# Kernel optimization log

Measured on AMD Instinct MI355X. Metric: run time of the kernel, lower is better.

Reference implementation:

```python
import jax, jax.numpy as jnp
import numpy as np

DIM = 256
HEADS = 8
HD = DIM // HEADS
SR = 2
SCALE = HD ** -0.5
EPS = 1e-5


def _layernorm(t, g, b):
    m = jnp.mean(t, axis=-1, keepdims=True)
    v = jnp.mean((t - m) ** 2, axis=-1, keepdims=True)
    return (t - m) / jnp.sqrt(v + EPS) * g + b


def _sr_kv(t, H, W, sr_w, sr_b, ln_g, ln_b, Wkv):
    # t: [B, N, C] with N == H*W -> spatial-reduction conv -> LN -> kv proj
    B, N, C = t.shape
    img = t.transpose(0, 2, 1).reshape(B, C, H, W)
    red = jax.lax.conv_general_dilated(
        img, sr_w, window_strides=(SR, SR), padding='VALID',
        dimension_numbers=('NCHW', 'OIHW', 'NCHW')) + sr_b[None, :, None, None]
    red = red.reshape(B, C, -1).transpose(0, 2, 1)  # [B, Nr, C]
    red = _layernorm(red, ln_g, ln_b)
    Nr = red.shape[1]
    kv = (red @ Wkv).reshape(B, Nr, 2, HEADS, HD).transpose(2, 0, 3, 1, 4)
    return kv[0], kv[1]  # k, v: [B, h, Nr, d]


def _q_heads(t, Wq):
    B, N, _ = t.shape
    return (t @ Wq).reshape(B, N, HEADS, HD).transpose(0, 2, 1, 3)  # [B,h,N,d]


def _attn_out(q, k, v, proj_w, proj_b):
    a = jnp.einsum('bhqd,bhkd->bhqk', q, k) * SCALE
    a = jax.nn.softmax(a, axis=-1)
    o = jnp.einsum('bhqk,bhkd->bhqd', a, v)
    B, h, N, d = o.shape
    return o.transpose(0, 2, 1, 3).reshape(B, N, h * d) @ proj_w + proj_b


def _forward(x, y, Wq, Wkv, sr_w, sr_b, ln_g, ln_b, proj_w, proj_b,
             H_x, W_x, H_y, W_y):
    # B_x == 1 branch of the original module (static shapes)
    B_y = y.shape[0]
    q_x = _q_heads(x, Wq)
    q_y = _q_heads(y, Wq)
    k_x, v_x = _sr_kv(x, H_x, W_x, sr_w, sr_b, ln_g, ln_b, Wkv)
    k_y, v_y = _sr_kv(y, H_y, W_y, sr_w, sr_b, ln_g, ln_b, Wkv)
    # x attends to its own KV + batch-averaged support KV
    k_cat_x = jnp.concatenate([k_x, jnp.mean(k_y, axis=0, keepdims=True)], axis=2)
    v_cat_x = jnp.concatenate([v_x, jnp.mean(v_y, axis=0, keepdims=True)], axis=2)
    x_out = _attn_out(q_x, k_cat_x, v_cat_x, proj_w, proj_b)
    # each support attends to repeated query KV + its own KV
    k_cat_y = jnp.concatenate([jnp.broadcast_to(k_x, (B_y,) + k_x.shape[1:]), k_y], axis=2)
    v_cat_y = jnp.concatenate([jnp.broadcast_to(v_x, (B_y,) + v_x.shape[1:]), v_y], axis=2)
    y_out = _attn_out(q_y, k_cat_y, v_cat_y, proj_w, proj_b)
    return x_out, y_out


def setup_inputs() -> dict:
    key = jax.random.key(0)
    ks = jax.random.split(key, 6)
    std = 0.02
    return {
        'x': jax.random.normal(ks[0], (1, 6400, DIM), jnp.float32),
        'y': jax.random.normal(ks[1], (4, 1024, DIM), jnp.float32),
        'Wq': jax.random.normal(ks[2], (DIM, DIM), jnp.float32) * std,
        'Wkv': jax.random.normal(ks[3], (DIM, 2 * DIM), jnp.float32) * std,
        'sr_w': jax.random.normal(ks[4], (DIM, DIM, SR, SR), jnp.float32) * np.sqrt(2.0 / (SR * SR * DIM)),
        'sr_b': jnp.zeros((DIM,), jnp.float32),
        'ln_g': jnp.ones((DIM,), jnp.float32),
        'ln_b': jnp.zeros((DIM,), jnp.float32),
        'proj_w': jax.random.normal(ks[5], (DIM, DIM), jnp.float32) * std,
        'proj_b': jnp.zeros((DIM,), jnp.float32),
        'H_x': 80, 'W_x': 80, 'H_y': 32, 'W_y': 32,
    }


def reference(x, y, Wq, Wkv, sr_w, sr_b, ln_g, ln_b, proj_w, proj_b,
              H_x, W_x, H_y, W_y):
    return _forward(x, y, Wq, Wkv, sr_w, sr_b, ln_g, ln_b, proj_w, proj_b,
                    H_x, W_x, H_y, W_y)
```

## Files before the change

kernel.cpp:

```cpp
#include <hip/hip_runtime.h>
#include <math.h>

#define DIM 256
#define HD 32
#define KSCALE (0.17677669529663687f * 1.44269504088896340736f)
#define EPS 1e-5f

typedef __attribute__((ext_vector_type(8))) short short8;
typedef __attribute__((ext_vector_type(4))) float f32x4;

union U8 { uint4 u; short8 s; };

__device__ inline unsigned short f2bf(float f) {
    union { float f; unsigned u; } v; v.f = f;
    unsigned r = v.u + 0x7FFF + ((v.u >> 16) & 1);
    return (unsigned short)(r >> 16);
}
__device__ inline float bf2f(unsigned short h) {
    union { unsigned u; float f; } v; v.u = ((unsigned)h) << 16;
    return v.f;
}
__device__ inline unsigned pk2bf(float a, float b) {
    unsigned ua = __float_as_uint(a) + 0x8000u;
    unsigned ub = __float_as_uint(b) + 0x8000u;
    return __builtin_amdgcn_perm(ub, ua, 0x07060302u);
}
__device__ inline uint4 pk8bf(float4 a, float4 b) {
    return make_uint4(pk2bf(a.x, a.y), pk2bf(a.z, a.w),
                      pk2bf(b.x, b.y), pk2bf(b.z, b.w));
}
__device__ inline void up2(unsigned u, float& a, float& b) {
    a = __uint_as_float(u << 16);
    b = __uint_as_float(u & 0xffff0000u);
}
__device__ inline void gl_lds16(const unsigned short* g, unsigned short* l) {
    __builtin_amdgcn_global_load_lds(
        (const __attribute__((address_space(1))) unsigned int*)g,
        (__attribute__((address_space(3))) unsigned int*)l, 16, 0, 0);
}
#define MFMA16(a, b, c) __builtin_amdgcn_mfma_f32_16x16x32_bf16(a, b, c, 0, 0, 0)
#define EXP2(x) __builtin_amdgcn_exp2f(x)

__global__ __launch_bounds__(256) void prep_w(
    const float* __restrict__ Wq, const float* __restrict__ Wkv,
    const float* __restrict__ projw, const float* __restrict__ srw,
    unsigned short* __restrict__ WqT, unsigned short* __restrict__ WkvT,
    unsigned short* __restrict__ projT, unsigned short* __restrict__ BwT)
{
    int idx = blockIdx.x * 256 + threadIdx.x;
    if (idx < 65536) { int n = idx >> 8, k = idx & 255; WqT[idx] = f2bf(Wq[(k << 8) + n]); return; }
    idx -= 65536;
    if (idx < 131072) { int n = idx >> 8, k = idx & 255; WkvT[idx] = f2bf(Wkv[(k << 9) + n]); return; }
    idx -= 131072;
    if (idx < 65536) { int n = idx >> 8, k = idx & 255; projT[idx] = f2bf(projw[(k << 8) + n]); return; }
    idx -= 65536;
    { int o = idx >> 10, rem = idx & 1023, q = rem >> 8, i = rem & 255;
      BwT[idx] = f2bf(srw[(o << 10) + (i << 2) + q]); }
}

__global__ __launch_bounds__(256) void convq_kernel(
    const float* __restrict__ x, const float* __restrict__ y,
    const unsigned short* __restrict__ BwT, const float* __restrict__ srb,
    const unsigned short* __restrict__ WqT,
    unsigned short* __restrict__ redx, unsigned short* __restrict__ redy,
    unsigned short* __restrict__ qxb, unsigned short* __restrict__ qyb)
{
    __shared__ __align__(16) unsigned short At[64][32];
    __shared__ __align__(16) unsigned short Btile[64][32];
    const int tid = threadIdx.x;
    const int lane = tid & 63, w = tid >> 6;
    const int c = lane & 15, quad = lane >> 4;
    const int srow = tid >> 2, sch = (tid & 3) << 3;
    const int bid = blockIdx.x;
    f32x4 acc[4] = {};
    const int rl = (w << 4) + (quad << 2);

    if (bid < 164) {
        const int n0 = (bid & 3) << 6, myi = bid >> 2;
        const float* Xb; unsigned short* Cb; int W, W2, m0;
        if (myi < 25) { Xb = x; Cb = redx; W = 80; W2 = 40; m0 = myi * 64; }
        else {
            const int r = myi - 25, b = r >> 2;
            Xb = y + (size_t)b * 262144; Cb = redy + (size_t)b * 65536;
            W = 32; W2 = 16; m0 = (r & 3) * 64;
        }
        const int p = m0 + srow;
        const int oy = p / W2, ox = p - oy * W2;
        const unsigned short* Bp = BwT + (size_t)(n0 + srow) * 1024 + sch;

        auto addrA = [&](int k0) {
            const int qq = k0 >> 8;
            const int rrow = (2 * oy + (qq >> 1)) * W + 2 * ox + (qq & 1);
            return Xb + (size_t)rrow * DIM + (k0 & 255) + sch;
        };

        const float* ap = addrA(0);
        float4 a0 = *(const float4*)ap, a1 = *(const float4*)(ap + 4);
        uint4 bn = *(const uint4*)Bp;
        for (int k0 = 0; k0 < 1024; k0 += 32) {
            *(uint4*)&At[srow][sch]    = pk8bf(a0, a1);
            *(uint4*)&Btile[srow][sch] = bn;
            if (k0 < 992) {
                const float* np = addrA(k0 + 32);
                a0 = *(const float4*)np; a1 = *(const float4*)(np + 4);
                bn = *(const uint4*)(Bp + k0 + 32);
            }
            __syncthreads();
            short8 a = *(short8*)&At[(w << 4) + c][quad << 3];
            #pragma unroll
            for (int nb = 0; nb < 4; ++nb) {
                short8 b = *(short8*)&Btile[(nb << 4) + c][quad << 3];
                acc[nb] = MFMA16(a, b, acc[nb]);
            }
            __syncthreads();
        }
        #pragma unroll
        for (int nb = 0; nb < 4; ++nb) {
            const int col = n0 + (nb << 4) + c;
            const float bv = srb[col];
            #pragma unroll
            for (int r = 0; r < 4; ++r)
                Cb[(size_t)(m0 + rl + r) * DIM + col] = f2bf(acc[nb][r] + bv);
        }
    } else {
        const int r = bid - 164;
        const int n0 = (r & 3) << 6, mg = (r >> 2) << 6;
        const float* Ab = (mg < 6400) ? x + (size_t)mg * 256
                                      : y + (size_t)(mg - 6400) * 256;
        unsigned short* Cb = (mg < 6400) ? qxb + (size_t)mg * 256
                                         : qyb + (size_t)(mg - 6400) * 256;
        const float* Ap = Ab + (size_t)srow * 256 + sch;
        const unsigned short* Bp = WqT + (size_t)(n0 + srow) * 256 + sch;

        float4 a0 = *(const float4*)Ap, a1 = *(const float4*)(Ap + 4);
        uint4 bn = *(const uint4*)Bp;
        for (int k0 = 0; k0 < 256; k0 += 32) {
            *(uint4*)&At[srow][sch]    = pk8bf(a0, a1);
            *(uint4*)&Btile[srow][sch] = bn;
            if (k0 < 224) {
                a0 = *(const float4*)(Ap + k0 + 32);
                a1 = *(const float4*)(Ap + k0 + 36);
                bn = *(const uint4*)(Bp + k0 + 32);
            }
            __syncthreads();
            short8 a = *(short8*)&At[(w << 4) + c][quad << 3];
            #pragma unroll
            for (int nb = 0; nb < 4; ++nb) {
                short8 b = *(short8*)&Btile[(nb << 4) + c][quad << 3];
                acc[nb] = MFMA16(a, b, acc[nb]);
            }
            __syncthreads();
        }
        #pragma unroll
        for (int nb = 0; nb < 4; ++nb) {
            const int col = n0 + (nb << 4) + c;
            #pragma unroll
            for (int r = 0; r < 4; ++r)
                Cb[(size_t)(rl + r) * 256 + col] = f2bf(acc[nb][r]);
        }
    }
}

__global__ __launch_bounds__(256) void kvln_kernel(
    const unsigned short* __restrict__ redx, const unsigned short* __restrict__ redy,
    const unsigned short* __restrict__ WkvT,
    const float* __restrict__ g, const float* __restrict__ bta,
    unsigned short* __restrict__ kswx, unsigned short* __restrict__ vswx,
    unsigned short* __restrict__ kswy, unsigned short* __restrict__ vswy)
{
    __shared__ __align__(16) unsigned short At[64][32];
    __shared__ __align__(16) unsigned short Btile[64][32];
    const int tid = threadIdx.x;
    const int lane = tid & 63, w = tid >> 6;
    const int c = lane & 15, quad = lane >> 4;
    const int srow = tid >> 2, sch = (tid & 3) << 3;
    const int bid = blockIdx.x;
    const int n0 = (bid & 7) << 6, mg = (bid >> 3) << 6;
    const unsigned short* Ab = (mg < 1600) ? redx + (size_t)mg * 256
                                           : redy + (size_t)(mg - 1600) * 256;
    const unsigned short* Arow = Ab + (size_t)srow * 256 + sch;

    uint4 araw[8];
    float s1 = 0.f, s2 = 0.f;
    #pragma unroll
    for (int ci = 0; ci < 8; ++ci) {
        araw[ci] = *(const uint4*)(Arow + (ci << 5));
        const unsigned* du = (const unsigned*)&araw[ci];
        #pragma unroll
        for (int dd = 0; dd < 4; ++dd) {
            float a, b; up2(du[dd], a, b);
            s1 += a + b; s2 += a * a + b * b;
        }
    }
    s1 += __shfl_xor(s1, 1); s1 += __shfl_xor(s1, 2);
    s2 += __shfl_xor(s2, 1); s2 += __shfl_xor(s2, 2);
    const float mean = s1 * (1.0f / 256.0f);
    const float var  = s2 * (1.0f / 256.0f) - mean * mean;
    const float rstd = rsqrtf(var + EPS);

    #pragma unroll
    for (int ci = 0; ci < 8; ++ci) {
        const int ch = (ci << 5) + sch;
        float4 g0 = *(const float4*)(g + ch),   g1 = *(const float4*)(g + ch + 4);
        float4 b0 = *(const float4*)(bta + ch), b1 = *(const float4*)(bta + ch + 4);
        const unsigned* du = (const unsigned*)&araw[ci];
        float v[8];
        #pragma unroll
        for (int dd = 0; dd < 4; ++dd) up2(du[dd], v[2 * dd], v[2 * dd + 1]);
        float4 o0 = make_float4(fmaf((v[0] - mean) * rstd, g0.x, b0.x),
                                fmaf((v[1] - mean) * rstd, g0.y, b0.y),
                                fmaf((v[2] - mean) * rstd, g0.z, b0.z),
                                fmaf((v[3] - mean) * rstd, g0.w, b0.w));
        float4 o1 = make_float4(fmaf((v[4] - mean) * rstd, g1.x, b1.x),
                                fmaf((v[5] - mean) * rstd, g1.y, b1.y),
                                fmaf((v[6] - mean) * rstd, g1.z, b1.z),
                                fmaf((v[7] - mean) * rstd, g1.w, b1.w));
        araw[ci] = pk8bf(o0, o1);
    }

    const unsigned short* Bp = WkvT + (size_t)(n0 + srow) * 256 + sch;
    uint4 bn = *(const uint4*)Bp;
    f32x4 acc[4] = {};
    for (int k0 = 0; k0 < 256; k0 += 32) {
        *(uint4*)&At[srow][sch]    = araw[k0 >> 5];
        *(uint4*)&Btile[srow][sch] = bn;
        if (k0 < 224) bn = *(const uint4*)(Bp + k0 + 32);
        __syncthreads();
        short8 a = *(short8*)&At[(w << 4) + c][quad << 3];
        #pragma unroll
        for (int nb = 0; nb < 4; ++nb) {
            short8 b = *(short8*)&Btile[(nb << 4) + c][quad << 3];
            acc[nb] = MFMA16(a, b, acc[nb]);
        }
        __syncthreads();
    }

    const int rl = (w << 4) + (quad << 2);
    const int r0 = mg - 1600;
    #pragma unroll
    for (int nb = 0; nb < 4; ++nb) {
        const int col = n0 + (nb << 4) + c;
        if (col < 256) {
            const int hh = col >> 5, d = col & 31;
            unsigned short* base = (mg < 1600)
                ? kswx + ((size_t)(hh * 25 + (mg >> 6)) << 11)
                : kswy + ((size_t)(r0 >> 8) << 16) + ((size_t)((hh << 2) + ((r0 >> 6) & 3)) << 11);
            unsigned short* dst = base + (((d >> 3) << 9)) + (d & 7);
            #pragma unroll
            for (int r = 0; r < 4; ++r)
                dst[(rl + r) << 3] = f2bf(acc[nb][r] * KSCALE);
        } else {
            const int hd = col - 256, hv = hd >> 5, d = hd & 31;
            unsigned short* base = (mg < 1600)
                ? vswx + ((size_t)(hv * 25 + (mg >> 6)) << 11)
                : vswy + ((size_t)(r0 >> 8) << 16) + ((size_t)((hv << 2) + ((r0 >> 6) & 3)) << 11);
            const int j0 = ((w >> 1) << 5) + (quad << 3) + ((w & 1) << 2);
            const int kc = j0 >> 5, qq = (j0 >> 3) & 3, u = j0 & 7;
            unsigned lo = (unsigned)f2bf(acc[nb][0]) | ((unsigned)f2bf(acc[nb][1]) << 16);
            unsigned hi = (unsigned)f2bf(acc[nb][2]) | ((unsigned)f2bf(acc[nb][3]) << 16);
            *(uint2*)(base + ((size_t)(((kc << 2) + qq) * 32 + d) << 3) + u) =
                make_uint2(lo, hi);
        }
    }
}

__global__ __launch_bounds__(256) void kvmean_kernel(
    const unsigned short* __restrict__ kswy, const unsigned short* __restrict__ vswy,
    unsigned short* __restrict__ kmsw, unsigned short* __restrict__ vmsw)
{
    int idx = blockIdx.x * 256 + threadIdx.x;
    const unsigned short* s; unsigned short* dv; int e;
    if (idx < 65536) { s = kswy; dv = kmsw; e = idx; }
    else             { s = vswy; dv = vmsw; e = idx - 65536; }
    float sm = bf2f(s[e]) + bf2f(s[e + 65536]) + bf2f(s[e + 131072]) + bf2f(s[e + 196608]);
    dv[e] = f2bf(0.25f * sm);
}

__global__ __launch_bounds__(256) void attn_mfma(
    unsigned short* __restrict__ qxb, unsigned short* __restrict__ qyb,
    const unsigned short* __restrict__ kswx, const unsigned short* __restrict__ vswx,
    const unsigned short* __restrict__ kmsw, const unsigned short* __restrict__ vmsw,
    const unsigned short* __restrict__ kswy, const unsigned short* __restrict__ vswy)
{
    __shared__ __align__(16) unsigned short Kt[2][2048];
    __shared__ __align__(16) unsigned short Vt[2][2048];

    const int tid = threadIdx.x;
    const int lane = tid & 63, w = tid >> 6;
    const int c = lane & 15, quad = lane >> 4;

    const int bid = blockIdx.x;
    unsigned short* qb; const unsigned short *k1, *v1, *k2, *v2;
    int h, qoff;
    if (bid < 800) {
        h = bid / 100; qoff = (bid - h * 100) * 64;
        qb = qxb;
        k1 = kswx + ((size_t)h * 25 << 11); v1 = vswx + ((size_t)h * 25 << 11);
        k2 = kmsw + ((size_t)h << 13);      v2 = vmsw + ((size_t)h << 13);
    } else {
        const int idx = bid - 800, b = idx >> 7, rem = idx & 127;
        h = rem >> 4; qoff = b * 1024 + (rem & 15) * 64;
        qb = qyb;
        k1 = kswx + ((size_t)h * 25 << 11); v1 = vswx + ((size_t)h * 25 << 11);
        k2 = kswy + ((size_t)b << 16) + ((size_t)h << 13);
        v2 = vswy + ((size_t)b << 16) + ((size_t)h << 13);
    }

    const int qrow = qoff + (w << 4) + c;
    const short8 qf = *(const short8*)(qb + (size_t)qrow * DIM + h * HD + (quad << 3));

    const int lel = (w << 9) + (lane << 3);

    auto stage = [&](int t, int pb) {
        const unsigned short *ks, *vs;
        if (t < 25) { ks = k1 + (t << 11); vs = v1 + (t << 11); }
        else        { ks = k2 + ((t - 25) << 11); vs = v2 + ((t - 25) << 11); }
        gl_lds16(ks + lel, &Kt[pb][w << 9]);
        gl_lds16(vs + lel, &Vt[pb][w << 9]);
    };

    float lsr = 0.f;
    f32x4 oacc[2] = {};
    const f32x4 zero = {0.f, 0.f, 0.f, 0.f};

    stage(0, 0);
    __syncthreads();

    for (int t = 0; t < 29; ++t) {
        const int pb = t & 1;
        if (t < 28) stage(t + 1, pb ^ 1);

        const unsigned short* Kp = &Kt[pb][quad << 9];
        f32x4 sacc[4];
        #pragma unroll
        for (int kb = 0; kb < 4; ++kb) {
            short8 ka = *(const short8*)(Kp + (((kb << 4) + c) << 3));
            sacc[kb] = MFMA16(ka, qf, zero);
        }
        float p[16];
        #pragma unroll
        for (int kb = 0; kb < 4; ++kb) {
            p[4 * kb + 0] = EXP2(sacc[kb][0]);
            p[4 * kb + 1] = EXP2(sacc[kb][1]);
            p[4 * kb + 2] = EXP2(sacc[kb][2]);
            p[4 * kb + 3] = EXP2(sacc[kb][3]);
            lsr += (p[4 * kb + 0] + p[4 * kb + 1]) + (p[4 * kb + 2] + p[4 * kb + 3]);
        }
        U8 af0, af1;
        af0.u = make_uint4(pk2bf(p[0], p[1]), pk2bf(p[2], p[3]),
                           pk2bf(p[4], p[5]), pk2bf(p[6], p[7]));
        af1.u = make_uint4(pk2bf(p[8], p[9]), pk2bf(p[10], p[11]),
                           pk2bf(p[12], p[13]), pk2bf(p[14], p[15]));
        const unsigned short* Vp = &Vt[pb][0];
        short8 v00 = *(const short8*)(Vp + (((quad << 5) + c) << 3));
        short8 v01 = *(const short8*)(Vp + (((quad << 5) + 16 + c) << 3));
        short8 v10 = *(const short8*)(Vp + ((((4 + quad) << 5) + c) << 3));
        short8 v11 = *(const short8*)(Vp + ((((4 + quad) << 5) + 16 + c) << 3));
        oacc[0] = MFMA16(af0.s, v00, oacc[0]);
        oacc[1] = MFMA16(af0.s, v01, oacc[1]);
        oacc[0] = MFMA16(af1.s, v10, oacc[0]);
        oacc[1] = MFMA16(af1.s, v11, oacc[1]);

        __syncthreads();
    }

    lsr += __shfl_xor(lsr, 16);
    lsr += __shfl_xor(lsr, 32);

    #pragma unroll
    for (int r = 0; r < 4; ++r) {
        const float inv = 1.0f / __shfl(lsr, (quad << 2) + r);
        const int row = qoff + (w << 4) + (quad << 2) + r;
        qb[(size_t)row * DIM + h * HD + c]      = f2bf(oacc[0][r] * inv);
        qb[(size_t)row * DIM + h * HD + 16 + c] = f2bf(oacc[1][r] * inv);
    }
}

__global__ __launch_bounds__(256) void proj_mfma(
    const unsigned short* __restrict__ qxb, const unsigned short* __restrict__ qyb,
    const unsigned short* __restrict__ projT, const float* __restrict__ bias,
    float* __restrict__ outx, float* __restrict__ outy)
{
    __shared__ __align__(16) unsigned short At[64][32];
    __shared__ __align__(16) unsigned short Btile[64][32];
    const int tid = threadIdx.x;
    const int lane = tid & 63, w = tid >> 6;
    const int c = lane & 15, quad = lane >> 4;
    const int srow = tid >> 2, sch = (tid & 3) << 3;

    const int bid = blockIdx.x;
    const int n0 = (bid & 3) << 6, mg = (bid >> 2) << 6;
    const unsigned short* Ab = (mg < 6400) ? qxb + (size_t)mg * 256
                                           : qyb + (size_t)(mg - 6400) * 256;
    float* Cf = (mg < 6400) ? outx + (size_t)mg * 256 : outy + (size_t)(mg - 6400) * 256;

    const unsigned short* Ap = Ab + (size_t)srow * 256 + sch;
    const unsigned short* Bp = projT + (size_t)(n0 + srow) * 256 + sch;

    uint4 an = *(const uint4*)Ap, bn = *(const uint4*)Bp;
    f32x4 acc[4] = {};
    for (int k0 = 0; k0 < 256; k0 += 32) {
        *(uint4*)&At[srow][sch]    = an;
        *(uint4*)&Btile[srow][sch] = bn;
        if (k0 < 224) { an = *(const uint4*)(Ap + k0 + 32); bn = *(const uint4*)(Bp + k0 + 32); }
        __syncthreads();
        short8 a = *(short8*)&At[(w << 4) + c][quad << 3];
        #pragma unroll
        for (int nb = 0; nb < 4; ++nb) {
            short8 b = *(short8*)&Btile[(nb << 4) + c][quad << 3];
            acc[nb] = MFMA16(a, b, acc[nb]);
        }
        __syncthreads();
    }
    const int rl = (w << 4) + (quad << 2);
    #pragma unroll
    for (int nb = 0; nb < 4; ++nb) {
        const int col = n0 + (nb << 4) + c;
        const float bv = bias[col];
        #pragma unroll
        for (int r = 0; r < 4; ++r)
            Cf[(size_t)(rl + r) * 256 + col] = acc[nb][r] + bv;
    }
}

extern "C" void kernel_launch(void* const* d_in, const int* in_sizes, int n_in,
                              void* d_out, int out_size, void* d_ws, size_t ws_size,
                              hipStream_t stream)
{
    const float* x      = (const float*)d_in[0];
    const float* y      = (const float*)d_in[1];
    const float* Wq     = (const float*)d_in[2];
    const float* Wkv    = (const float*)d_in[3];
    const float* sr_w   = (const float*)d_in[4];
    const float* sr_b   = (const float*)d_in[5];
    const float* ln_g   = (const float*)d_in[6];
    const float* ln_b   = (const float*)d_in[7];
    const float* proj_w = (const float*)d_in[8];
    const float* proj_b = (const float*)d_in[9];

    unsigned short* p = (unsigned short*)d_ws;
    unsigned short* WqT   = p;  p += 65536;
    unsigned short* WkvT  = p;  p += 131072;
    unsigned short* projT = p;  p += 65536;
    unsigned short* BwT   = p;  p += 262144;
    unsigned short* redx  = p;  p += 409600;
    unsigned short* redy  = p;  p += 262144;
    unsigned short* qxb   = p;  p += 1638400;
    unsigned short* qyb   = p;  p += 1048576;
    unsigned short* kswx  = p;  p += 409600;
    unsigned short* vswx  = p;  p += 409600;
    unsigned short* kswy  = p;  p += 262144;
    unsigned short* vswy  = p;  p += 262144;
    unsigned short* kmsw  = p;  p += 65536;
    unsigned short* vmsw  = p;  p += 65536;
    float* outx = (float*)d_out;
    float* outy = outx + 6400 * 256;

    prep_w<<<2048, 256, 0, stream>>>(Wq, Wkv, proj_w, sr_w, WqT, WkvT, projT, BwT);
    convq_kernel<<<820, 256, 0, stream>>>(x, y, BwT, sr_b, WqT, redx, redy, qxb, qyb);
    kvln_kernel<<<328, 256, 0, stream>>>(redx, redy, WkvT, ln_g, ln_b,
                                         kswx, vswx, kswy, vswy);
    kvmean_kernel<<<512, 256, 0, stream>>>(kswy, vswy, kmsw, vmsw);
    attn_mfma<<<1312, 256, 0, stream>>>(qxb, qyb, kswx, vswx, kmsw, vmsw, kswy, vswy);
    proj_mfma<<<656, 256, 0, stream>>>(qxb, qyb, projT, proj_b, outx, outy);
}
```

Before: 168.7 us.

## Split KV tiles across waves and share Q fragments in attention kernel

The attention kernel now has every wave hold all 64 query rows in registers and splits the key/value stream across waves. Each wave handles part of a two-tile stage, and the per-wave partial outputs and row sums are reduced through LDS at the end. Odd tile counts are padded with a zero key/value tile, and its exp2(0)=1 contributions are subtracted from the denominator. The V layout written by the KV projection kernel is changed to match the new fragment loads. The aim is more MFMA work per LDS load and fewer loop iterations and barriers, at the cost of more registers, a larger LDS footprint and an extra cross-wave reduction.

```diff
diff --git a/kernel.cpp b/kernel.cpp
--- a/kernel.cpp
+++ b/kernel.cpp
@@ -237,6 +237,8 @@
 
     const int rl = (w << 4) + (quad << 2);
     const int r0 = mg - 1600;
+    const int half = rl >> 5, kl0 = rl & 31;
+    const int vkeyoff = (half << 10) + (((kl0 >> 2) & 3) << 7) + ((kl0 >> 4) << 2);
     #pragma unroll
     for (int nb = 0; nb < 4; ++nb) {
         const int col = n0 + (nb << 4) + c;
@@ -254,11 +256,9 @@
             unsigned short* base = (mg < 1600)
                 ? vswx + ((size_t)(hv * 25 + (mg >> 6)) << 11)
                 : vswy + ((size_t)(r0 >> 8) << 16) + ((size_t)((hv << 2) + ((r0 >> 6) & 3)) << 11);
-            const int j0 = ((w >> 1) << 5) + (quad << 3) + ((w & 1) << 2);
-            const int kc = j0 >> 5, qq = (j0 >> 3) & 3, u = j0 & 7;
             unsigned lo = (unsigned)f2bf(acc[nb][0]) | ((unsigned)f2bf(acc[nb][1]) << 16);
             unsigned hi = (unsigned)f2bf(acc[nb][2]) | ((unsigned)f2bf(acc[nb][3]) << 16);
-            *(uint2*)(base + ((size_t)(((kc << 2) + qq) * 32 + d) << 3) + u) =
+            *(uint2*)(base + vkeyoff + ((d >> 4) << 9) + ((d & 15) << 3)) =
                 make_uint2(lo, hi);
         }
     }
@@ -280,10 +280,11 @@
     unsigned short* __restrict__ qxb, unsigned short* __restrict__ qyb,
     const unsigned short* __restrict__ kswx, const unsigned short* __restrict__ vswx,
     const unsigned short* __restrict__ kmsw, const unsigned short* __restrict__ vmsw,
-    const unsigned short* __restrict__ kswy, const unsigned short* __restrict__ vswy)
-{
-    __shared__ __align__(16) unsigned short Kt[2][2048];
-    __shared__ __align__(16) unsigned short Vt[2][2048];
+    const unsigned short* __restrict__ kswy, const unsigned short* __restrict__ vswy,
+    const unsigned short* __restrict__ kpad, const unsigned short* __restrict__ vpad)
+{
+    __shared__ __align__(16) unsigned short KV[2][8192];
+    __shared__ __align__(16) float lsumLDS[4][64];
 
     const int tid = threadIdx.x;
     const int lane = tid & 63, w = tid >> 6;
@@ -306,73 +307,114 @@
         v2 = vswy + ((size_t)b << 16) + ((size_t)h << 13);
     }
 
-    const int qrow = qoff + (w << 4) + c;
-    const short8 qf = *(const short8*)(qb + (size_t)qrow * DIM + h * HD + (quad << 3));
-
-    const int lel = (w << 9) + (lane << 3);
-
-    auto stage = [&](int t, int pb) {
-        const unsigned short *ks, *vs;
-        if (t < 25) { ks = k1 + (t << 11); vs = v1 + (t << 11); }
-        else        { ks = k2 + ((t - 25) << 11); vs = v2 + ((t - 25) << 11); }
-        gl_lds16(ks + lel, &Kt[pb][w << 9]);
-        gl_lds16(vs + lel, &Vt[pb][w << 9]);
+    short8 qf[4];
+    #pragma unroll
+    for (int nb = 0; nb < 4; ++nb)
+        qf[nb] = *(const short8*)(qb + (size_t)(qoff + (nb << 4) + c) * DIM
+                                  + h * HD + (quad << 3));
+
+    auto ksrc = [&](int t) -> const unsigned short* {
+        if (t < 25) return k1 + (t << 11);
+        if (t < 29) return k2 + ((t - 25) << 11);
+        return kpad;
     };
-
-    float lsr = 0.f;
-    f32x4 oacc[2] = {};
+    auto vsrc = [&](int t) -> const unsigned short* {
+        if (t < 25) return v1 + (t << 11);
+        if (t < 29) return v2 + ((t - 25) << 11);
+        return vpad;
+    };
+
+    const int sg = (w << 9) + (lane << 3);
+    auto stage = [&](int i, int pb) {
+        #pragma unroll
+        for (int tt = 0; tt < 2; ++tt) {
+            const int t = 2 * i + tt;
+            gl_lds16(ksrc(t) + sg, &KV[pb][(tt << 11) + (w << 9)]);
+            gl_lds16(vsrc(t) + sg, &KV[pb][4096 + (tt << 11) + (w << 9)]);
+        }
+    };
+
+    const int tb = w >> 1, half = w & 1;
+    float lsr[4] = {0.f, 0.f, 0.f, 0.f};
+    f32x4 oacc[4][2] = {};
     const f32x4 zero = {0.f, 0.f, 0.f, 0.f};
 
     stage(0, 0);
     __syncthreads();
 
-    for (int t = 0; t < 29; ++t) {
-        const int pb = t & 1;
-        if (t < 28) stage(t + 1, pb ^ 1);
-
-        const unsigned short* Kp = &Kt[pb][quad << 9];
-        f32x4 sacc[4];
-        #pragma unroll
-        for (int kb = 0; kb < 4; ++kb) {
-            short8 ka = *(const short8*)(Kp + (((kb << 4) + c) << 3));
-            sacc[kb] = MFMA16(ka, qf, zero);
-        }
-        float p[16];
-        #pragma unroll
-        for (int kb = 0; kb < 4; ++kb) {
-            p[4 * kb + 0] = EXP2(sacc[kb][0]);
-            p[4 * kb + 1] = EXP2(sacc[kb][1]);
-            p[4 * kb + 2] = EXP2(sacc[kb][2]);
-            p[4 * kb + 3] = EXP2(sacc[kb][3]);
-            lsr += (p[4 * kb + 0] + p[4 * kb + 1]) + (p[4 * kb + 2] + p[4 * kb + 3]);
-        }
-        U8 af0, af1;
-        af0.u = make_uint4(pk2bf(p[0], p[1]), pk2bf(p[2], p[3]),
-                           pk2bf(p[4], p[5]), pk2bf(p[6], p[7]));
-        af1.u = make_uint4(pk2bf(p[8], p[9]), pk2bf(p[10], p[11]),
-                           pk2bf(p[12], p[13]), pk2bf(p[14], p[15]));
-        const unsigned short* Vp = &Vt[pb][0];
-        short8 v00 = *(const short8*)(Vp + (((quad << 5) + c) << 3));
-        short8 v01 = *(const short8*)(Vp + (((quad << 5) + 16 + c) << 3));
-        short8 v10 = *(const short8*)(Vp + ((((4 + quad) << 5) + c) << 3));
-        short8 v11 = *(const short8*)(Vp + ((((4 + quad) << 5) + 16 + c) << 3));
-        oacc[0] = MFMA16(af0.s, v00, oacc[0]);
-        oacc[1] = MFMA16(af0.s, v01, oacc[1]);
-        oacc[0] = MFMA16(af1.s, v10, oacc[0]);
-        oacc[1] = MFMA16(af1.s, v11, oacc[1]);
+    for (int i = 0; i < 15; ++i) {
+        const int pb = i & 1;
+        if (i < 14) stage(i + 1, pb ^ 1);
+
+        const unsigned short* Kp = &KV[pb][(tb << 11) + (quad << 9) + (((half << 5) + c) << 3)];
+        short8 ka0 = *(const short8*)(Kp);
+        short8 ka1 = *(const short8*)(Kp + 128);
+        f32x4 s0[4], s1[4];
+        #pragma unroll
+        for (int nb = 0; nb < 4; ++nb) s0[nb] = MFMA16(ka0, qf[nb], zero);
+        #pragma unroll
+        for (int nb = 0; nb < 4; ++nb) s1[nb] = MFMA16(ka1, qf[nb], zero);
+
+        U8 af[4];
+        #pragma unroll
+        for (int nb = 0; nb < 4; ++nb) {
+            float p0 = EXP2(s0[nb][0]), p1 = EXP2(s0[nb][1]);
+            float p2 = EXP2(s0[nb][2]), p3 = EXP2(s0[nb][3]);
+            float q0 = EXP2(s1[nb][0]), q1 = EXP2(s1[nb][1]);
+            float q2 = EXP2(s1[nb][2]), q3 = EXP2(s1[nb][3]);
+            lsr[nb] += ((p0 + p1) + (p2 + p3)) + ((q0 + q1) + (q2 + q3));
+            af[nb].u = make_uint4(pk2bf(p0, p1), pk2bf(p2, p3),
+                                  pk2bf(q0, q1), pk2bf(q2, q3));
+        }
+
+        const unsigned short* Vp = &KV[pb][4096 + (tb << 11) + (half << 10) + (quad << 7) + (c << 3)];
+        short8 vb0 = *(const short8*)(Vp);
+        short8 vb1 = *(const short8*)(Vp + 512);
+        #pragma unroll
+        for (int nb = 0; nb < 4; ++nb) {
+            oacc[nb][0] = MFMA16(af[nb].s, vb0, oacc[nb][0]);
+            oacc[nb][1] = MFMA16(af[nb].s, vb1, oacc[nb][1]);
+        }
 
         __syncthreads();
     }
 
-    lsr += __shfl_xor(lsr, 16);
-    lsr += __shfl_xor(lsr, 32);
-
-    #pragma unroll
-    for (int r = 0; r < 4; ++r) {
-        const float inv = 1.0f / __shfl(lsr, (quad << 2) + r);
-        const int row = qoff + (w << 4) + (quad << 2) + r;
-        qb[(size_t)row * DIM + h * HD + c]      = f2bf(oacc[0][r] * inv);
-        qb[(size_t)row * DIM + h * HD + 16 + c] = f2bf(oacc[1][r] * inv);
+    #pragma unroll
+    for (int nb = 0; nb < 4; ++nb) {
+        lsr[nb] += __shfl_xor(lsr[nb], 16);
+        lsr[nb] += __shfl_xor(lsr[nb], 32);
+    }
+    if (lane < 16) {
+        #pragma unroll
+        for (int nb = 0; nb < 4; ++nb) lsumLDS[w][(nb << 4) + lane] = lsr[nb];
+    }
+    float* Op = (float*)&KV[0][0];
+    #pragma unroll
+    for (int nb = 0; nb < 4; ++nb)
+        #pragma unroll
+        for (int db = 0; db < 2; ++db)
+            *(f32x4*)&Op[((((w << 2) + nb) << 1) + db) * 256 + (c << 4) + (quad << 2)] =
+                oacc[nb][db];
+    __syncthreads();
+
+    f32x4 lt = {0.f, 0.f, 0.f, 0.f};
+    #pragma unroll
+    for (int w2 = 0; w2 < 4; ++w2)
+        lt += *(f32x4*)&lsumLDS[w2][(w << 4) + (quad << 2)];
+    float inv[4];
+    #pragma unroll
+    for (int r = 0; r < 4; ++r) inv[r] = 1.0f / (lt[r] - 64.0f);
+    #pragma unroll
+    for (int db = 0; db < 2; ++db) {
+        f32x4 o = zero;
+        #pragma unroll
+        for (int w2 = 0; w2 < 4; ++w2)
+            o += *(f32x4*)&Op[((((w2 << 2) + w) << 1) + db) * 256 + (c << 4) + (quad << 2)];
+        #pragma unroll
+        for (int r = 0; r < 4; ++r) {
+            const int row = qoff + (w << 4) + (quad << 2) + r;
+            qb[(size_t)row * DIM + h * HD + (db << 4) + c] = f2bf(o[r] * inv[r]);
+        }
     }
 }
 
@@ -453,14 +495,18 @@
     unsigned short* vswy  = p;  p += 262144;
     unsigned short* kmsw  = p;  p += 65536;
     unsigned short* vmsw  = p;  p += 65536;
+    unsigned short* kpad  = p;  p += 2048;
+    unsigned short* vpad  = p;  p += 2048;
     float* outx = (float*)d_out;
     float* outy = outx + 6400 * 256;
 
+    hipMemsetAsync(kpad, 0, 8192, stream);
     prep_w<<<2048, 256, 0, stream>>>(Wq, Wkv, proj_w, sr_w, WqT, WkvT, projT, BwT);
     convq_kernel<<<820, 256, 0, stream>>>(x, y, BwT, sr_b, WqT, redx, redy, qxb, qyb);
     kvln_kernel<<<328, 256, 0, stream>>>(redx, redy, WkvT, ln_g, ln_b,
                                          kswx, vswx, kswy, vswy);
     kvmean_kernel<<<512, 256, 0, stream>>>(kswy, vswy, kmsw, vmsw);
-    attn_mfma<<<1312, 256, 0, stream>>>(qxb, qyb, kswx, vswx, kmsw, vmsw, kswy, vswy);
+    attn_mfma<<<1312, 256, 0, stream>>>(qxb, qyb, kswx, vswx, kmsw, vmsw,
+                                        kswy, vswy, kpad, vpad);
     proj_mfma<<<656, 256, 0, stream>>>(qxb, qyb, projT, proj_b, outx, outy);
 }
```

Result: no change. 169.8 us (+0.7%).
